# Optimization experiments

Hardware: AMD Instinct MI355X
Metric: run time of the kernel (lower is better)

## Reference

```python
import jax, jax.numpy as jnp
import numpy as np

B, C_IN, C_OUT, HID, HW = 128, 1024, 1024, 256, 32

def setup_inputs() -> dict:
    key = jax.random.key(0)
    ks = jax.random.split(key, 5)
    inp = {
        "input": jax.random.normal(ks[0], (B, C_IN, HW, HW), dtype=jnp.float32),
        "fc1_w": jax.random.normal(ks[1], (HID, C_IN), dtype=jnp.float32) * 0.02,
        "fc1_b": jnp.ones((HID,), dtype=jnp.float32),
        "fc2_w": jax.random.normal(ks[2], (C_OUT, HID), dtype=jnp.float32) * (np.sqrt(2.0 / HID)),
        "fc2_b": jnp.ones((C_OUT,), dtype=jnp.float32),
        "noise": jax.random.normal(ks[3], (B, C_OUT), dtype=jnp.float32),
        "swap_idx": jax.random.randint(ks[4], (C_OUT // 2,), 0, B, dtype=jnp.int64 if jax.config.read('jax_enable_x64') else jnp.int32),
    }
    return inp

def reference(input, fc1_w, fc1_b, fc2_w, fc2_b, noise, swap_idx):
    # global average pool over H, W -> [B, C_in]
    x = jnp.mean(input, axis=(2, 3))
    y = jax.nn.relu(x @ fc1_w.T + fc1_b)          # [B, HID]
    y2 = y @ fc2_w.T + fc2_b                      # [B, C_out]
    g = noise + y2
    v1 = jnp.clip(1.2 * jax.nn.sigmoid(g) - 0.1, 0.0, 1.0)
    v2 = (g > 0).astype(v1.dtype)
    # semhash: overwrite random batch rows of v1 with hard-binarized v2
    swapped = v1.at[swap_idx].set(v2[swap_idx])
    # straight-through: forward uses swapped values, backward is identity w.r.t. v1
    out = v1 + jax.lax.stop_gradient(swapped - v1)
    return out[:, :, None, None]                  # [B, C_out, 1, 1]
```

## Files before the change

### kernel.cpp

```cpp
#include <hip/hip_runtime.h>
#include <cstdint>

#define NB    128
#define NCIN  1024
#define NCOUT 1024
#define NHID  256
#define NHW   1024

typedef float f32x4 __attribute__((ext_vector_type(4)));

__global__ __launch_bounds__(256) void gap_kernel(const float* __restrict__ in,
                                                  float* __restrict__ x) {
    const int wave = (blockIdx.x * 256 + threadIdx.x) >> 6;
    const int lane = threadIdx.x & 63;
    const int row0 = wave * 4;
    const f32x4* base = reinterpret_cast<const f32x4*>(in);
#pragma unroll
    for (int r = 0; r < 4; ++r) {
        const f32x4* p = base + (size_t)(row0 + r) * (NHW / 4);
        f32x4 v0 = __builtin_nontemporal_load(p + lane);
        f32x4 v1 = __builtin_nontemporal_load(p + lane + 64);
        f32x4 v2 = __builtin_nontemporal_load(p + lane + 128);
        f32x4 v3 = __builtin_nontemporal_load(p + lane + 192);
        float t0 = (v0.x + v0.y) + (v0.z + v0.w);
        float t1 = (v1.x + v1.y) + (v1.z + v1.w);
        float t2 = (v2.x + v2.y) + (v2.z + v2.w);
        float t3 = (v3.x + v3.y) + (v3.z + v3.w);
        double s = ((double)t0 + (double)t1) + ((double)t2 + (double)t3);
#pragma unroll
        for (int off = 32; off > 0; off >>= 1)
            s += __shfl_down(s, off, 64);
        if (lane == 0) x[row0 + r] = (float)(s * (1.0 / 1024.0));
    }
}

__global__ __launch_bounds__(256) void fc1_kernel(const float* __restrict__ x,
                                                  const float* __restrict__ w1,
                                                  const float* __restrict__ b1,
                                                  float* __restrict__ y) {
    __shared__ float  xs[NCIN];
    __shared__ double part[64][4];
    const int b  = blockIdx.x >> 2;
    const int hq = blockIdx.x & 3;
    const int t  = threadIdx.x;

    reinterpret_cast<float4*>(xs)[t] =
        reinterpret_cast<const float4*>(x + (size_t)b * NCIN)[t];
    __syncthreads();

    const int hl = t & 63;
    const int cs = t >> 6;
    const int h  = hq * 64 + hl;
    const float4* w  = reinterpret_cast<const float4*>(w1 + (size_t)h * NCIN + cs * 256);
    const float*  xp = xs + cs * 256;
    double a0 = 0.0, a1 = 0.0, a2 = 0.0, a3 = 0.0;
#pragma unroll 8
    for (int i = 0; i < 64; ++i) {
        float4 wv = w[i];
        a0 += (double)wv.x * (double)xp[4 * i + 0];
        a1 += (double)wv.y * (double)xp[4 * i + 1];
        a2 += (double)wv.z * (double)xp[4 * i + 2];
        a3 += (double)wv.w * (double)xp[4 * i + 3];
    }
    part[hl][cs] = (a0 + a1) + (a2 + a3);
    __syncthreads();

    if (t < 64) {
        double v = ((part[t][0] + part[t][1]) + (part[t][2] + part[t][3]))
                 + (double)b1[hq * 64 + t];
        y[(size_t)b * NHID + hq * 64 + t] = (float)(v > 0.0 ? v : 0.0);
    }
}

__global__ __launch_bounds__(256) void fc2_kernel(const float* __restrict__ y,
                                                  const float* __restrict__ w2,
                                                  const float* __restrict__ b2,
                                                  const float* __restrict__ noise,
                                                  const int* __restrict__ swap_idx,
                                                  int n_swap,
                                                  float* __restrict__ out) {
    __shared__ float ys[NHID];
    __shared__ int flag;
    const int b  = blockIdx.x >> 2;
    const int jq = blockIdx.x & 3;
    const int t  = threadIdx.x;

    if (t == 0) flag = 0;
    ys[t] = y[(size_t)b * NHID + t];
    __syncthreads();
    for (int i = t; i < n_swap; i += 256)
        if (swap_idx[i] == b) flag = 1;
    __syncthreads();
    const bool sw = (flag != 0);

    const int j = jq * 256 + t;
    const float4* w = reinterpret_cast<const float4*>(w2 + (size_t)j * NHID);
    double a0 = 0.0, a1 = 0.0, a2 = 0.0, a3 = 0.0;
#pragma unroll 8
    for (int i = 0; i < NHID / 4; ++i) {
        float4 wv = w[i];
        a0 += (double)wv.x * (double)ys[4 * i + 0];
        a1 += (double)wv.y * (double)ys[4 * i + 1];
        a2 += (double)wv.z * (double)ys[4 * i + 2];
        a3 += (double)wv.w * (double)ys[4 * i + 3];
    }
    double g = ((a0 + a1) + (a2 + a3)) + (double)b2[j]
             + (double)noise[(size_t)b * NCOUT + j];
    float gf  = (float)g;
    float sig = 1.0f / (1.0f + __expf(-gf));
    float v1  = fminf(fmaxf(1.2f * sig - 0.1f, 0.0f), 1.0f);
    float v2  = (g > 0.0) ? 1.0f : 0.0f;
    out[(size_t)b * NCOUT + j] = sw ? v2 : v1;
}

extern "C" void kernel_launch(void* const* d_in, const int* in_sizes, int n_in,
                              void* d_out, int out_size, void* d_ws, size_t ws_size,
                              hipStream_t stream) {
    const float* input = (const float*)d_in[0];
    const float* fc1_w = (const float*)d_in[1];
    const float* fc1_b = (const float*)d_in[2];
    const float* fc2_w = (const float*)d_in[3];
    const float* fc2_b = (const float*)d_in[4];
    const float* noise = (const float*)d_in[5];
    const int*   swap  = (const int*)d_in[6];
    const int n_swap = in_sizes[6];

    float* x = (float*)d_ws;
    float* y = x + NB * NCIN;

    gap_kernel<<<(NB * NCIN) / 16, 256, 0, stream>>>(input, x);
    fc1_kernel<<<NB * 4, 256, 0, stream>>>(x, fc1_w, fc1_b, y);
    fc2_kernel<<<NB * 4, 256, 0, stream>>>(y, fc2_w, fc2_b, noise, swap, n_swap,
                                           (float*)d_out);
}
```

Measured before the change: 119.0 us.

## Prefetch FC weights into cache during GAP and split FC work over more blocks

Adds 16 extra blocks to the pooling kernel that read fc1/fc2 weights and the noise tensor, so those arrays are already cache-resident when the FC kernels run. The FC kernels now split each output's dot product across 8 threads (fc1) or 2 threads (fc2) with shuffle reductions, and use twice as many blocks. Per-thread weight reads become shorter and more parallel, which targets the latency-bound FC stages. The warm blocks compete with the bandwidth-bound pooling stream and may not keep the data in cache until the next launch.

```diff
diff --git a/kernel.cpp b/kernel.cpp
--- a/kernel.cpp
+++ b/kernel.cpp
@@ -7,11 +7,36 @@
 #define NHID  256
 #define NHW   1024
 
+#define WARM_BLOCKS 16
+#define GAP_BLOCKS  ((NB * NCIN) / 16)
+
 typedef float f32x4 __attribute__((ext_vector_type(4)));
 
 __global__ __launch_bounds__(256) void gap_kernel(const float* __restrict__ in,
-                                                  float* __restrict__ x) {
-    const int wave = (blockIdx.x * 256 + threadIdx.x) >> 6;
+                                                  float* __restrict__ x,
+                                                  const float* __restrict__ w1,
+                                                  const float* __restrict__ w2,
+                                                  const float* __restrict__ noise) {
+    if (blockIdx.x < WARM_BLOCKS) {
+        const int start = blockIdx.x * 256 + threadIdx.x;
+        float acc = 0.f;
+        const float4* p1 = reinterpret_cast<const float4*>(w1);
+        const float4* p2 = reinterpret_cast<const float4*>(w2);
+        const float4* pn = reinterpret_cast<const float4*>(noise);
+        for (int i = start; i < (NHID * NCIN) / 4; i += WARM_BLOCKS * 256) {
+            float4 v = p1[i]; acc += (v.x + v.y) + (v.z + v.w);
+        }
+        for (int i = start; i < (NCOUT * NHID) / 4; i += WARM_BLOCKS * 256) {
+            float4 v = p2[i]; acc += (v.x + v.y) + (v.z + v.w);
+        }
+        for (int i = start; i < (NB * NCOUT) / 4; i += WARM_BLOCKS * 256) {
+            float4 v = pn[i]; acc += (v.x + v.y) + (v.z + v.w);
+        }
+        asm volatile("" :: "v"(acc));
+        return;
+    }
+
+    const int wave = ((blockIdx.x - WARM_BLOCKS) * 256 + threadIdx.x) >> 6;
     const int lane = threadIdx.x & 63;
     const int row0 = wave * 4;
     const f32x4* base = reinterpret_cast<const f32x4*>(in);
@@ -38,37 +63,38 @@
                                                   const float* __restrict__ w1,
                                                   const float* __restrict__ b1,
                                                   float* __restrict__ y) {
-    __shared__ float  xs[NCIN];
-    __shared__ double part[64][4];
-    const int b  = blockIdx.x >> 2;
-    const int hq = blockIdx.x & 3;
+    __shared__ float4 xs4[8][33];
+    const int b  = blockIdx.x >> 3;
+    const int ho = blockIdx.x & 7;
     const int t  = threadIdx.x;
 
-    reinterpret_cast<float4*>(xs)[t] =
-        reinterpret_cast<const float4*>(x + (size_t)b * NCIN)[t];
+    {
+        float4 v = reinterpret_cast<const float4*>(x + (size_t)b * NCIN)[t];
+        xs4[t >> 5][t & 31] = v;
+    }
     __syncthreads();
 
-    const int hl = t & 63;
-    const int cs = t >> 6;
-    const int h  = hq * 64 + hl;
-    const float4* w  = reinterpret_cast<const float4*>(w1 + (size_t)h * NCIN + cs * 256);
-    const float*  xp = xs + cs * 256;
+    const int hl = t >> 3;
+    const int cs = t & 7;
+    const int h  = ho * 32 + hl;
+    const float4* w = reinterpret_cast<const float4*>(w1 + (size_t)h * NCIN + cs * 128);
     double a0 = 0.0, a1 = 0.0, a2 = 0.0, a3 = 0.0;
-#pragma unroll 8
-    for (int i = 0; i < 64; ++i) {
+#pragma unroll
+    for (int i = 0; i < 32; ++i) {
         float4 wv = w[i];
-        a0 += (double)wv.x * (double)xp[4 * i + 0];
-        a1 += (double)wv.y * (double)xp[4 * i + 1];
-        a2 += (double)wv.z * (double)xp[4 * i + 2];
-        a3 += (double)wv.w * (double)xp[4 * i + 3];
+        float4 xv = xs4[cs][i];
+        a0 += (double)wv.x * (double)xv.x;
+        a1 += (double)wv.y * (double)xv.y;
+        a2 += (double)wv.z * (double)xv.z;
+        a3 += (double)wv.w * (double)xv.w;
     }
-    part[hl][cs] = (a0 + a1) + (a2 + a3);
-    __syncthreads();
-
-    if (t < 64) {
-        double v = ((part[t][0] + part[t][1]) + (part[t][2] + part[t][3]))
-                 + (double)b1[hq * 64 + t];
-        y[(size_t)b * NHID + hq * 64 + t] = (float)(v > 0.0 ? v : 0.0);
+    double s = (a0 + a1) + (a2 + a3);
+    s += __shfl_xor(s, 1, 64);
+    s += __shfl_xor(s, 2, 64);
+    s += __shfl_xor(s, 4, 64);
+    if (cs == 0) {
+        double v = s + (double)b1[h];
+        y[(size_t)b * NHID + h] = (float)(v > 0.0 ? v : 0.0);
     }
 }
 
@@ -81,8 +107,8 @@
                                                   float* __restrict__ out) {
     __shared__ float ys[NHID];
     __shared__ int flag;
-    const int b  = blockIdx.x >> 2;
-    const int jq = blockIdx.x & 3;
+    const int b  = blockIdx.x >> 3;
+    const int jo = blockIdx.x & 7;
     const int t  = threadIdx.x;
 
     if (t == 0) flag = 0;
@@ -93,24 +119,30 @@
     __syncthreads();
     const bool sw = (flag != 0);
 
-    const int j = jq * 256 + t;
-    const float4* w = reinterpret_cast<const float4*>(w2 + (size_t)j * NHID);
+    const int jl = t >> 1;
+    const int ch = t & 1;
+    const int j  = jo * 128 + jl;
+    const float4* w  = reinterpret_cast<const float4*>(w2 + (size_t)j * NHID + ch * 128);
+    const float*  yp = ys + ch * 128;
     double a0 = 0.0, a1 = 0.0, a2 = 0.0, a3 = 0.0;
-#pragma unroll 8
-    for (int i = 0; i < NHID / 4; ++i) {
+#pragma unroll
+    for (int i = 0; i < 32; ++i) {
         float4 wv = w[i];
-        a0 += (double)wv.x * (double)ys[4 * i + 0];
-        a1 += (double)wv.y * (double)ys[4 * i + 1];
-        a2 += (double)wv.z * (double)ys[4 * i + 2];
-        a3 += (double)wv.w * (double)ys[4 * i + 3];
+        a0 += (double)wv.x * (double)yp[4 * i + 0];
+        a1 += (double)wv.y * (double)yp[4 * i + 1];
+        a2 += (double)wv.z * (double)yp[4 * i + 2];
+        a3 += (double)wv.w * (double)yp[4 * i + 3];
     }
-    double g = ((a0 + a1) + (a2 + a3)) + (double)b2[j]
-             + (double)noise[(size_t)b * NCOUT + j];
-    float gf  = (float)g;
-    float sig = 1.0f / (1.0f + __expf(-gf));
-    float v1  = fminf(fmaxf(1.2f * sig - 0.1f, 0.0f), 1.0f);
-    float v2  = (g > 0.0) ? 1.0f : 0.0f;
-    out[(size_t)b * NCOUT + j] = sw ? v2 : v1;
+    double s = (a0 + a1) + (a2 + a3);
+    s += __shfl_xor(s, 1, 64);
+    if (ch == 0) {
+        double g = s + (double)b2[j] + (double)noise[(size_t)b * NCOUT + j];
+        float gf  = (float)g;
+        float sig = 1.0f / (1.0f + __expf(-gf));
+        float v1  = fminf(fmaxf(1.2f * sig - 0.1f, 0.0f), 1.0f);
+        float v2  = (g > 0.0) ? 1.0f : 0.0f;
+        out[(size_t)b * NCOUT + j] = sw ? v2 : v1;
+    }
 }
 
 extern "C" void kernel_launch(void* const* d_in, const int* in_sizes, int n_in,
@@ -128,8 +160,9 @@
     float* x = (float*)d_ws;
     float* y = x + NB * NCIN;
 
-    gap_kernel<<<(NB * NCIN) / 16, 256, 0, stream>>>(input, x);
-    fc1_kernel<<<NB * 4, 256, 0, stream>>>(x, fc1_w, fc1_b, y);
-    fc2_kernel<<<NB * 4, 256, 0, stream>>>(y, fc2_w, fc2_b, noise, swap, n_swap,
+    gap_kernel<<<WARM_BLOCKS + GAP_BLOCKS, 256, 0, stream>>>(input, x, fc1_w,
+                                                             fc2_w, noise);
+    fc1_kernel<<<NB * 8, 256, 0, stream>>>(x, fc1_w, fc1_b, y);
+    fc2_kernel<<<NB * 8, 256, 0, stream>>>(y, fc2_w, fc2_b, noise, swap, n_swap,
                                            (float*)d_out);
 }
```

After: 119.0 us. Within noise of the previous version (-0.0%).

## Fuse fc1 and fc2 into one per-batch kernel and restructure pooling

Applied to the files above, without the earlier changes.

Merges the fc1 and fc2 kernels into a single kernel with one block per batch row, so the hidden activations stay in shared memory and one launch plus a global round trip are removed. The pooling kernel now issues all eight loads per thread up front and reduces through shared memory across 8 rows per block, with twice as many blocks. In exchange, the fused MLP launches only 128 blocks, each thread runs a serial 1024-long fp64 dot product for fc1, and the fc2 weight rows are read with strided per-thread access, so it may underfill the GPU and run longer.

```diff
diff --git a/kernel.cpp b/kernel.cpp
--- a/kernel.cpp
+++ b/kernel.cpp
@@ -11,106 +11,101 @@
 
 __global__ __launch_bounds__(256) void gap_kernel(const float* __restrict__ in,
                                                   float* __restrict__ x) {
-    const int wave = (blockIdx.x * 256 + threadIdx.x) >> 6;
+    __shared__ float part[8][65];
+    const int w    = threadIdx.x >> 6;
     const int lane = threadIdx.x & 63;
-    const int row0 = wave * 4;
+    const int rowBase = blockIdx.x * 8;
     const f32x4* base = reinterpret_cast<const f32x4*>(in);
+
+    f32x4 v[2][4];
 #pragma unroll
-    for (int r = 0; r < 4; ++r) {
-        const f32x4* p = base + (size_t)(row0 + r) * (NHW / 4);
-        f32x4 v0 = __builtin_nontemporal_load(p + lane);
-        f32x4 v1 = __builtin_nontemporal_load(p + lane + 64);
-        f32x4 v2 = __builtin_nontemporal_load(p + lane + 128);
-        f32x4 v3 = __builtin_nontemporal_load(p + lane + 192);
-        float t0 = (v0.x + v0.y) + (v0.z + v0.w);
-        float t1 = (v1.x + v1.y) + (v1.z + v1.w);
-        float t2 = (v2.x + v2.y) + (v2.z + v2.w);
-        float t3 = (v3.x + v3.y) + (v3.z + v3.w);
-        double s = ((double)t0 + (double)t1) + ((double)t2 + (double)t3);
+    for (int r = 0; r < 2; ++r) {
+        const f32x4* p = base + (size_t)(rowBase + w * 2 + r) * (NHW / 4);
 #pragma unroll
-        for (int off = 32; off > 0; off >>= 1)
-            s += __shfl_down(s, off, 64);
-        if (lane == 0) x[row0 + r] = (float)(s * (1.0 / 1024.0));
+        for (int k = 0; k < 4; ++k)
+            v[r][k] = __builtin_nontemporal_load(p + lane + 64 * k);
     }
+#pragma unroll
+    for (int r = 0; r < 2; ++r) {
+        float t0 = (v[r][0].x + v[r][0].y) + (v[r][0].z + v[r][0].w);
+        float t1 = (v[r][1].x + v[r][1].y) + (v[r][1].z + v[r][1].w);
+        float t2 = (v[r][2].x + v[r][2].y) + (v[r][2].z + v[r][2].w);
+        float t3 = (v[r][3].x + v[r][3].y) + (v[r][3].z + v[r][3].w);
+        part[w * 2 + r][lane] = (t0 + t1) + (t2 + t3);
+    }
+    __syncthreads();
+
+    const int row = threadIdx.x >> 5;
+    const int k   = threadIdx.x & 31;
+    double s = (double)part[row][k] + (double)part[row][k + 32];
+    s += __shfl_xor(s, 1, 64);
+    s += __shfl_xor(s, 2, 64);
+    s += __shfl_xor(s, 4, 64);
+    s += __shfl_xor(s, 8, 64);
+    s += __shfl_xor(s, 16, 64);
+    if (k == 0) x[rowBase + row] = (float)(s * (1.0 / 1024.0));
 }
 
-__global__ __launch_bounds__(256) void fc1_kernel(const float* __restrict__ x,
+__global__ __launch_bounds__(256) void mlp_kernel(const float* __restrict__ x,
                                                   const float* __restrict__ w1,
                                                   const float* __restrict__ b1,
-                                                  float* __restrict__ y) {
-    __shared__ float  xs[NCIN];
-    __shared__ double part[64][4];
-    const int b  = blockIdx.x >> 2;
-    const int hq = blockIdx.x & 3;
-    const int t  = threadIdx.x;
-
-    reinterpret_cast<float4*>(xs)[t] =
-        reinterpret_cast<const float4*>(x + (size_t)b * NCIN)[t];
-    __syncthreads();
-
-    const int hl = t & 63;
-    const int cs = t >> 6;
-    const int h  = hq * 64 + hl;
-    const float4* w  = reinterpret_cast<const float4*>(w1 + (size_t)h * NCIN + cs * 256);
-    const float*  xp = xs + cs * 256;
-    double a0 = 0.0, a1 = 0.0, a2 = 0.0, a3 = 0.0;
-#pragma unroll 8
-    for (int i = 0; i < 64; ++i) {
-        float4 wv = w[i];
-        a0 += (double)wv.x * (double)xp[4 * i + 0];
-        a1 += (double)wv.y * (double)xp[4 * i + 1];
-        a2 += (double)wv.z * (double)xp[4 * i + 2];
-        a3 += (double)wv.w * (double)xp[4 * i + 3];
-    }
-    part[hl][cs] = (a0 + a1) + (a2 + a3);
-    __syncthreads();
-
-    if (t < 64) {
-        double v = ((part[t][0] + part[t][1]) + (part[t][2] + part[t][3]))
-                 + (double)b1[hq * 64 + t];
-        y[(size_t)b * NHID + hq * 64 + t] = (float)(v > 0.0 ? v : 0.0);
-    }
-}
-
-__global__ __launch_bounds__(256) void fc2_kernel(const float* __restrict__ y,
                                                   const float* __restrict__ w2,
                                                   const float* __restrict__ b2,
                                                   const float* __restrict__ noise,
                                                   const int* __restrict__ swap_idx,
                                                   int n_swap,
                                                   float* __restrict__ out) {
+    __shared__ float xs[NCIN];
     __shared__ float ys[NHID];
     __shared__ int flag;
-    const int b  = blockIdx.x >> 2;
-    const int jq = blockIdx.x & 3;
-    const int t  = threadIdx.x;
+    const int b = blockIdx.x;
+    const int t = threadIdx.x;
 
     if (t == 0) flag = 0;
-    ys[t] = y[(size_t)b * NHID + t];
+    reinterpret_cast<float4*>(xs)[t] =
+        reinterpret_cast<const float4*>(x + (size_t)b * NCIN)[t];
     __syncthreads();
     for (int i = t; i < n_swap; i += 256)
         if (swap_idx[i] == b) flag = 1;
+
+    {
+        const float4* w = reinterpret_cast<const float4*>(w1 + (size_t)t * NCIN);
+        double a0 = 0.0, a1 = 0.0, a2 = 0.0, a3 = 0.0;
+#pragma unroll 8
+        for (int i = 0; i < NCIN / 4; ++i) {
+            float4 wv = w[i];
+            a0 += (double)wv.x * (double)xs[4 * i + 0];
+            a1 += (double)wv.y * (double)xs[4 * i + 1];
+            a2 += (double)wv.z * (double)xs[4 * i + 2];
+            a3 += (double)wv.w * (double)xs[4 * i + 3];
+        }
+        double v = ((a0 + a1) + (a2 + a3)) + (double)b1[t];
+        ys[t] = (float)(v > 0.0 ? v : 0.0);
+    }
     __syncthreads();
     const bool sw = (flag != 0);
 
-    const int j = jq * 256 + t;
-    const float4* w = reinterpret_cast<const float4*>(w2 + (size_t)j * NHID);
-    double a0 = 0.0, a1 = 0.0, a2 = 0.0, a3 = 0.0;
+#pragma unroll
+    for (int kk = 0; kk < NCOUT / 256; ++kk) {
+        const int j = kk * 256 + t;
+        const float4* w = reinterpret_cast<const float4*>(w2 + (size_t)j * NHID);
+        double c0 = 0.0, c1 = 0.0, c2 = 0.0, c3 = 0.0;
 #pragma unroll 8
-    for (int i = 0; i < NHID / 4; ++i) {
-        float4 wv = w[i];
-        a0 += (double)wv.x * (double)ys[4 * i + 0];
-        a1 += (double)wv.y * (double)ys[4 * i + 1];
-        a2 += (double)wv.z * (double)ys[4 * i + 2];
-        a3 += (double)wv.w * (double)ys[4 * i + 3];
+        for (int i = 0; i < NHID / 4; ++i) {
+            float4 wv = w[i];
+            c0 += (double)wv.x * (double)ys[4 * i + 0];
+            c1 += (double)wv.y * (double)ys[4 * i + 1];
+            c2 += (double)wv.z * (double)ys[4 * i + 2];
+            c3 += (double)wv.w * (double)ys[4 * i + 3];
+        }
+        double g = ((c0 + c1) + (c2 + c3)) + (double)b2[j]
+                 + (double)noise[(size_t)b * NCOUT + j];
+        float gf  = (float)g;
+        float sig = 1.0f / (1.0f + __expf(-gf));
+        float v1  = fminf(fmaxf(1.2f * sig - 0.1f, 0.0f), 1.0f);
+        float v2  = (g > 0.0) ? 1.0f : 0.0f;
+        out[(size_t)b * NCOUT + j] = sw ? v2 : v1;
     }
-    double g = ((a0 + a1) + (a2 + a3)) + (double)b2[j]
-             + (double)noise[(size_t)b * NCOUT + j];
-    float gf  = (float)g;
-    float sig = 1.0f / (1.0f + __expf(-gf));
-    float v1  = fminf(fmaxf(1.2f * sig - 0.1f, 0.0f), 1.0f);
-    float v2  = (g > 0.0) ? 1.0f : 0.0f;
-    out[(size_t)b * NCOUT + j] = sw ? v2 : v1;
 }
 
 extern "C" void kernel_launch(void* const* d_in, const int* in_sizes, int n_in,
@@ -126,10 +121,8 @@
     const int n_swap = in_sizes[6];
 
     float* x = (float*)d_ws;
-    float* y = x + NB * NCIN;
 
-    gap_kernel<<<(NB * NCIN) / 16, 256, 0, stream>>>(input, x);
-    fc1_kernel<<<NB * 4, 256, 0, stream>>>(x, fc1_w, fc1_b, y);
-    fc2_kernel<<<NB * 4, 256, 0, stream>>>(y, fc2_w, fc2_b, noise, swap, n_swap,
-                                           (float*)d_out);
+    gap_kernel<<<(NB * NCIN) / 8, 256, 0, stream>>>(input, x);
+    mlp_kernel<<<NB, 256, 0, stream>>>(x, fc1_w, fc1_b, fc2_w, fc2_b,
+                                       noise, swap, n_swap, (float*)d_out);
 }
```

New measurement: 149.1 us. 1.25x slower.
